# Kernel tuning notes

Measured on AMD Instinct MI355X. Metric: run time of the kernel, lower is better.

Reference implementation:

```python
import jax, jax.numpy as jnp
import numpy as np

N_E = 1024
E_DIM = 64
BETA = 0.25
N_TOK = 262144


def setup_inputs() -> dict:
    key = jax.random.key(0)
    k1, k2 = jax.random.split(key)
    x = jax.random.normal(k1, (N_TOK, E_DIM), dtype=jnp.float32)
    # torch init: uniform(-1/n_e, 1/n_e); use same distribution for the codebook
    codebook = jax.random.uniform(k2, (N_E, E_DIM), dtype=jnp.float32,
                                  minval=-1.0 / N_E, maxval=1.0 / N_E)
    return {"x": x, "codebook": codebook}


def reference(x, codebook):
    latent = x.reshape(-1, E_DIM)                       # [N, e_dim]
    # squared euclidean distances: [N, n_e]
    d = (jnp.sum(latent * latent, axis=1, keepdims=True)
         + jnp.sum(codebook * codebook, axis=1)[None, :]
         - 2.0 * jnp.matmul(latent, codebook.T))
    indices = jnp.argmin(d, axis=-1)                    # [N] int
    x_q = jnp.take(codebook, indices, axis=0).reshape(x.shape)
    # commitment: mse(stop_grad(x_q), x); codebook: mse(x_q, stop_grad(x))
    diff2 = jnp.mean((x_q - x) ** 2)
    loss = diff2 + BETA * diff2  # fwd values identical; grads differ (handled in bwd module)
    # straight-through estimator
    x_q_st = x + jax.lax.stop_gradient(x_q - x)
    return x_q_st, loss, indices.reshape(x.shape[:-1])
```

## Files before the change

### kernel.cpp

```cpp
#include <hip/hip_runtime.h>
#include <float.h>

#define N_TOK 262144
#define N_E   1024
#define E_DIM 64
#define BETA  0.25f

typedef float f32x64 __attribute__((ext_vector_type(64)));

__device__ __forceinline__ float np_sumsq64_v(f32x64 v)
{
    float r0 = __fmul_rn(v[1], v[1]);
    float r1 = __fmul_rn(v[2], v[2]);
    float r2 = __fmul_rn(v[3], v[3]);
    float r3 = __fmul_rn(v[4], v[4]);
    float r4 = __fmul_rn(v[5], v[5]);
    float r5 = __fmul_rn(v[6], v[6]);
    float r6 = __fmul_rn(v[7], v[7]);
    float r7 = __fmul_rn(v[8], v[8]);
#define VQ_ACC8(blk)                                                     \
    r0 = __fadd_rn(r0, __fmul_rn(v[1 + (blk) + 0], v[1 + (blk) + 0]));  \
    r1 = __fadd_rn(r1, __fmul_rn(v[1 + (blk) + 1], v[1 + (blk) + 1]));  \
    r2 = __fadd_rn(r2, __fmul_rn(v[1 + (blk) + 2], v[1 + (blk) + 2]));  \
    r3 = __fadd_rn(r3, __fmul_rn(v[1 + (blk) + 3], v[1 + (blk) + 3]));  \
    r4 = __fadd_rn(r4, __fmul_rn(v[1 + (blk) + 4], v[1 + (blk) + 4]));  \
    r5 = __fadd_rn(r5, __fmul_rn(v[1 + (blk) + 5], v[1 + (blk) + 5]));  \
    r6 = __fadd_rn(r6, __fmul_rn(v[1 + (blk) + 6], v[1 + (blk) + 6]));  \
    r7 = __fadd_rn(r7, __fmul_rn(v[1 + (blk) + 7], v[1 + (blk) + 7]))
    VQ_ACC8(8);
    VQ_ACC8(16);
    VQ_ACC8(24);
    VQ_ACC8(32);
    VQ_ACC8(40);
    VQ_ACC8(48);
#undef VQ_ACC8
    float tA  = __fadd_rn(__fadd_rn(r0, r1), __fadd_rn(r2, r3));
    float tB  = __fadd_rn(__fadd_rn(r4, r5), __fadd_rn(r6, r7));
    float res = __fadd_rn(tA, tB);
    res = __fadd_rn(res, __fmul_rn(v[57], v[57]));
    res = __fadd_rn(res, __fmul_rn(v[58], v[58]));
    res = __fadd_rn(res, __fmul_rn(v[59], v[59]));
    res = __fadd_rn(res, __fmul_rn(v[60], v[60]));
    res = __fadd_rn(res, __fmul_rn(v[61], v[61]));
    res = __fadd_rn(res, __fmul_rn(v[62], v[62]));
    res = __fadd_rn(res, __fmul_rn(v[63], v[63]));
    return __fadd_rn(__fmul_rn(v[0], v[0]), res);
}

__global__ __launch_bounds__(256) void vq_prep(const float* __restrict__ cb,
                                               float* __restrict__ scn,
                                               float* __restrict__ loss_slot)
{
    int j = blockIdx.x * 256 + threadIdx.x;
    if (j < N_E) {
        const float* c = cb + (size_t)j * E_DIM;
        f32x64 cr;
#pragma unroll
        for (int k = 0; k < E_DIM; k += 4) {
            float4 v = *(const float4*)(c + k);
            cr[k] = v.x; cr[k + 1] = v.y; cr[k + 2] = v.z; cr[k + 3] = v.w;
        }
        scn[j] = np_sumsq64_v(cr);
    }
    if (blockIdx.x == 0 && threadIdx.x == 0) *loss_slot = 0.f;
}

__global__ __launch_bounds__(256)
void vq_main(const float* __restrict__ x,
             const float* __restrict__ cb,
             const float* __restrict__ scn,
             float* __restrict__ xq_out,
             float* __restrict__ loss_out,
             float* __restrict__ idx_out)
{
    const int tok = blockIdx.x * blockDim.x + threadIdx.x;

    f32x64 xr;
    {
        const float* xrow = x + (size_t)tok * E_DIM;
#pragma unroll
        for (int k = 0; k < E_DIM; k += 4) {
            float4 v = *(const float4*)(xrow + k);
            xr[k] = v.x; xr[k + 1] = v.y; xr[k + 2] = v.z; xr[k + 3] = v.w;
        }
    }

    const float sx = np_sumsq64_v(xr);

    float dmin = FLT_MAX;
    int   imin = 0;

    for (int j = 0; j < N_E; j += 2) {
        const float* c0 = cb + (size_t)j * E_DIM;
        const float* c1 = c0 + E_DIM;
        float m0 = 0.f, m1 = 0.f;
#pragma unroll
        for (int k = 0; k < E_DIM; ++k) {
            m0 = fmaf(xr[k], c0[k], m0);
            m1 = fmaf(xr[k], c1[k], m1);
        }
        float d0 = __fsub_rn(__fadd_rn(sx, scn[j    ]), __fmul_rn(2.0f, m0));
        float d1 = __fsub_rn(__fadd_rn(sx, scn[j + 1]), __fmul_rn(2.0f, m1));
        if (d0 < dmin) { dmin = d0; imin = j; }
        if (d1 < dmin) { dmin = d1; imin = j + 1; }
    }

    float lsum = 0.f;
    {
        const float* cmin = cb + (size_t)imin * E_DIM;
        float*       xq   = xq_out + (size_t)tok * E_DIM;
#pragma unroll
        for (int k = 0; k < E_DIM; k += 4) {
            float4 cv = *(const float4*)(cmin + k);
            *(float4*)(xq + k) = cv;
            float e0 = cv.x - xr[k    ];
            float e1 = cv.y - xr[k + 1];
            float e2 = cv.z - xr[k + 2];
            float e3 = cv.w - xr[k + 3];
            lsum = fmaf(e0, e0, lsum);
            lsum = fmaf(e1, e1, lsum);
            lsum = fmaf(e2, e2, lsum);
            lsum = fmaf(e3, e3, lsum);
        }
    }
    idx_out[tok] = (float)imin;

    for (int m = 1; m < 64; m <<= 1) lsum += __shfl_xor(lsum, m, 64);
    __shared__ float red[4];
    const int lane = threadIdx.x & 63;
    const int wid  = threadIdx.x >> 6;
    if (lane == 0) red[wid] = lsum;
    __syncthreads();
    if (threadIdx.x == 0) {
        float part = red[0] + red[1] + red[2] + red[3];
        const float scale = (1.0f + BETA) / ((float)N_TOK * (float)E_DIM);
        atomicAdd(loss_out, part * scale);
    }
}

extern "C" void kernel_launch(void* const* d_in, const int* in_sizes, int n_in,
                              void* d_out, int out_size, void* d_ws, size_t ws_size,
                              hipStream_t stream)
{
    const float* x  = (const float*)d_in[0];
    const float* cb = (const float*)d_in[1];

    float* out  = (float*)d_out;
    float* xq   = out;
    float* loss = out + (size_t)N_TOK * E_DIM;
    float* idx  = loss + 1;

    float* scn = (float*)d_ws;

    vq_prep<<<N_E / 256, 256, 0, stream>>>(cb, scn, loss);
    vq_main<<<N_TOK / 256, 256, 0, stream>>>(x, cb, scn, xq, loss, idx);
}
```

Baseline: 614.5 us.

## Stage token rows in shared memory and tile codebook into 16-entry register blocks

Each token's vector now lives in a transposed shared-memory tile instead of 64 registers, and the distance loop computes 16 codebook dot products at once over 16-wide k-chunks. This is meant to free registers for more resident waves and to amortise each x value across 16 codewords, which raises FMA density per load. The block size also drops from 256 to 128. In exchange every x element is re-read from LDS for each codebook tile, and the codebook loads, which are uniform across the wave, become 16 separate scalar or broadcast streams.

```diff
diff --git a/kernel.cpp b/kernel.cpp
--- a/kernel.cpp
+++ b/kernel.cpp
@@ -5,6 +5,8 @@
 #define N_E   1024
 #define E_DIM 64
 #define BETA  0.25f
+#define BLK   128
+#define NTILE 16
 
 typedef float f32x64 __attribute__((ext_vector_type(64)));
 
@@ -19,20 +21,15 @@
     float r6 = __fmul_rn(v[7], v[7]);
     float r7 = __fmul_rn(v[8], v[8]);
 #define VQ_ACC8(blk)                                                     \
-    r0 = __fadd_rn(r0, __fmul_rn(v[1 + (blk) + 0], v[1 + (blk) + 0]));  \
-    r1 = __fadd_rn(r1, __fmul_rn(v[1 + (blk) + 1], v[1 + (blk) + 1]));  \
-    r2 = __fadd_rn(r2, __fmul_rn(v[1 + (blk) + 2], v[1 + (blk) + 2]));  \
-    r3 = __fadd_rn(r3, __fmul_rn(v[1 + (blk) + 3], v[1 + (blk) + 3]));  \
-    r4 = __fadd_rn(r4, __fmul_rn(v[1 + (blk) + 4], v[1 + (blk) + 4]));  \
-    r5 = __fadd_rn(r5, __fmul_rn(v[1 + (blk) + 5], v[1 + (blk) + 5]));  \
-    r6 = __fadd_rn(r6, __fmul_rn(v[1 + (blk) + 6], v[1 + (blk) + 6]));  \
-    r7 = __fadd_rn(r7, __fmul_rn(v[1 + (blk) + 7], v[1 + (blk) + 7]))
-    VQ_ACC8(8);
-    VQ_ACC8(16);
-    VQ_ACC8(24);
-    VQ_ACC8(32);
-    VQ_ACC8(40);
-    VQ_ACC8(48);
+    r0 = __fadd_rn(r0, __fmul_rn(v[1 + (blk)], v[1 + (blk)]));          \
+    r1 = __fadd_rn(r1, __fmul_rn(v[2 + (blk)], v[2 + (blk)]));          \
+    r2 = __fadd_rn(r2, __fmul_rn(v[3 + (blk)], v[3 + (blk)]));          \
+    r3 = __fadd_rn(r3, __fmul_rn(v[4 + (blk)], v[4 + (blk)]));          \
+    r4 = __fadd_rn(r4, __fmul_rn(v[5 + (blk)], v[5 + (blk)]));          \
+    r5 = __fadd_rn(r5, __fmul_rn(v[6 + (blk)], v[6 + (blk)]));          \
+    r6 = __fadd_rn(r6, __fmul_rn(v[7 + (blk)], v[7 + (blk)]));          \
+    r7 = __fadd_rn(r7, __fmul_rn(v[8 + (blk)], v[8 + (blk)]))
+    VQ_ACC8(8); VQ_ACC8(16); VQ_ACC8(24); VQ_ACC8(32); VQ_ACC8(40); VQ_ACC8(48);
 #undef VQ_ACC8
     float tA  = __fadd_rn(__fadd_rn(r0, r1), __fadd_rn(r2, r3));
     float tB  = __fadd_rn(__fadd_rn(r4, r5), __fadd_rn(r6, r7));
@@ -65,7 +62,7 @@
     if (blockIdx.x == 0 && threadIdx.x == 0) *loss_slot = 0.f;
 }
 
-__global__ __launch_bounds__(256)
+__global__ __launch_bounds__(BLK)
 void vq_main(const float* __restrict__ x,
              const float* __restrict__ cb,
              const float* __restrict__ scn,
@@ -73,36 +70,110 @@
              float* __restrict__ loss_out,
              float* __restrict__ idx_out)
 {
-    const int tok = blockIdx.x * blockDim.x + threadIdx.x;
-
-    f32x64 xr;
+    __shared__ float At[E_DIM][BLK];
+    __shared__ float red[2];
+
+    const int t   = threadIdx.x;
+    const int tok = blockIdx.x * BLK + t;
+
+#define XT(k) At[(k)][t]
+
     {
         const float* xrow = x + (size_t)tok * E_DIM;
 #pragma unroll
-        for (int k = 0; k < E_DIM; k += 4) {
-            float4 v = *(const float4*)(xrow + k);
-            xr[k] = v.x; xr[k + 1] = v.y; xr[k + 2] = v.z; xr[k + 3] = v.w;
+        for (int c = 0; c < 16; ++c) {
+            float4 v = *(const float4*)(xrow + 4 * c);
+            At[4 * c + 0][t] = v.x;
+            At[4 * c + 1][t] = v.y;
+            At[4 * c + 2][t] = v.z;
+            At[4 * c + 3][t] = v.w;
         }
     }
 
-    const float sx = np_sumsq64_v(xr);
+    float sx;
+    {
+#define Q(k) __fmul_rn(XT(k), XT(k))
+        float r0 = Q(1), r1 = Q(2), r2 = Q(3), r3 = Q(4);
+        float r4 = Q(5), r5 = Q(6), r6 = Q(7), r7 = Q(8);
+#define SACC(b)                                  \
+        r0 = __fadd_rn(r0, Q(1 + (b)));          \
+        r1 = __fadd_rn(r1, Q(2 + (b)));          \
+        r2 = __fadd_rn(r2, Q(3 + (b)));          \
+        r3 = __fadd_rn(r3, Q(4 + (b)));          \
+        r4 = __fadd_rn(r4, Q(5 + (b)));          \
+        r5 = __fadd_rn(r5, Q(6 + (b)));          \
+        r6 = __fadd_rn(r6, Q(7 + (b)));          \
+        r7 = __fadd_rn(r7, Q(8 + (b)));
+        SACC(8) SACC(16) SACC(24) SACC(32) SACC(40) SACC(48)
+#undef SACC
+        float tA  = __fadd_rn(__fadd_rn(r0, r1), __fadd_rn(r2, r3));
+        float tB  = __fadd_rn(__fadd_rn(r4, r5), __fadd_rn(r6, r7));
+        float res = __fadd_rn(tA, tB);
+        res = __fadd_rn(res, Q(57));
+        res = __fadd_rn(res, Q(58));
+        res = __fadd_rn(res, Q(59));
+        res = __fadd_rn(res, Q(60));
+        res = __fadd_rn(res, Q(61));
+        res = __fadd_rn(res, Q(62));
+        res = __fadd_rn(res, Q(63));
+        sx = __fadd_rn(Q(0), res);
+#undef Q
+    }
 
     float dmin = FLT_MAX;
     int   imin = 0;
 
-    for (int j = 0; j < N_E; j += 2) {
-        const float* c0 = cb + (size_t)j * E_DIM;
-        const float* c1 = c0 + E_DIM;
-        float m0 = 0.f, m1 = 0.f;
-#pragma unroll
-        for (int k = 0; k < E_DIM; ++k) {
-            m0 = fmaf(xr[k], c0[k], m0);
-            m1 = fmaf(xr[k], c1[k], m1);
-        }
-        float d0 = __fsub_rn(__fadd_rn(sx, scn[j    ]), __fmul_rn(2.0f, m0));
-        float d1 = __fsub_rn(__fadd_rn(sx, scn[j + 1]), __fmul_rn(2.0f, m1));
-        if (d0 < dmin) { dmin = d0; imin = j; }
-        if (d1 < dmin) { dmin = d1; imin = j + 1; }
+#define FMAQ(xv, kk, ma, mb, mc, md)             \
+    ma = fmaf(xv, p0[kk], ma);                   \
+    mb = fmaf(xv, p1[kk], mb);                   \
+    mc = fmaf(xv, p2[kk], mc);                   \
+    md = fmaf(xv, p3[kk], md);
+
+#define GROUP(jbase, kc, ma, mb, mc, md) do {                        \
+    const float* p0 = cb + (size_t)(jbase) * E_DIM + (kc);           \
+    const float* p1 = p0 + E_DIM;                                    \
+    const float* p2 = p1 + E_DIM;                                    \
+    const float* p3 = p2 + E_DIM;                                    \
+    FMAQ(x0, 0, ma, mb, mc, md)  FMAQ(x1, 1, ma, mb, mc, md)         \
+    FMAQ(x2, 2, ma, mb, mc, md)  FMAQ(x3, 3, ma, mb, mc, md)         \
+    FMAQ(x4, 4, ma, mb, mc, md)  FMAQ(x5, 5, ma, mb, mc, md)         \
+    FMAQ(x6, 6, ma, mb, mc, md)  FMAQ(x7, 7, ma, mb, mc, md)         \
+    FMAQ(x8, 8, ma, mb, mc, md)  FMAQ(x9, 9, ma, mb, mc, md)         \
+    FMAQ(x10, 10, ma, mb, mc, md) FMAQ(x11, 11, ma, mb, mc, md)      \
+    FMAQ(x12, 12, ma, mb, mc, md) FMAQ(x13, 13, ma, mb, mc, md)      \
+    FMAQ(x14, 14, ma, mb, mc, md) FMAQ(x15, 15, ma, mb, mc, md)      \
+} while (0)
+
+#define CHUNK(kc) do {                                               \
+    const float x0  = XT((kc) + 0),  x1  = XT((kc) + 1);             \
+    const float x2  = XT((kc) + 2),  x3  = XT((kc) + 3);             \
+    const float x4  = XT((kc) + 4),  x5  = XT((kc) + 5);             \
+    const float x6  = XT((kc) + 6),  x7  = XT((kc) + 7);             \
+    const float x8  = XT((kc) + 8),  x9  = XT((kc) + 9);             \
+    const float x10 = XT((kc) + 10), x11 = XT((kc) + 11);            \
+    const float x12 = XT((kc) + 12), x13 = XT((kc) + 13);            \
+    const float x14 = XT((kc) + 14), x15 = XT((kc) + 15);            \
+    GROUP(j0 + 0,  (kc), m00, m01, m02, m03);                        \
+    GROUP(j0 + 4,  (kc), m04, m05, m06, m07);                        \
+    GROUP(j0 + 8,  (kc), m08, m09, m10, m11);                        \
+    GROUP(j0 + 12, (kc), m12, m13, m14, m15);                        \
+} while (0)
+
+#define DCHK(jl, mv) {                                                      \
+    float d = __fsub_rn(__fadd_rn(sx, scn[j0 + (jl)]), __fmul_rn(2.0f, mv)); \
+    if (d < dmin) { dmin = d; imin = j0 + (jl); }                           \
+}
+
+    for (int j0 = 0; j0 < N_E; j0 += NTILE) {
+        float m00 = 0.f, m01 = 0.f, m02 = 0.f, m03 = 0.f;
+        float m04 = 0.f, m05 = 0.f, m06 = 0.f, m07 = 0.f;
+        float m08 = 0.f, m09 = 0.f, m10 = 0.f, m11 = 0.f;
+        float m12 = 0.f, m13 = 0.f, m14 = 0.f, m15 = 0.f;
+        CHUNK(0); CHUNK(16); CHUNK(32); CHUNK(48);
+        DCHK(0, m00)  DCHK(1, m01)  DCHK(2, m02)  DCHK(3, m03)
+        DCHK(4, m04)  DCHK(5, m05)  DCHK(6, m06)  DCHK(7, m07)
+        DCHK(8, m08)  DCHK(9, m09)  DCHK(10, m10) DCHK(11, m11)
+        DCHK(12, m12) DCHK(13, m13) DCHK(14, m14) DCHK(15, m15)
     }
 
     float lsum = 0.f;
@@ -110,13 +181,13 @@
         const float* cmin = cb + (size_t)imin * E_DIM;
         float*       xq   = xq_out + (size_t)tok * E_DIM;
 #pragma unroll
-        for (int k = 0; k < E_DIM; k += 4) {
-            float4 cv = *(const float4*)(cmin + k);
-            *(float4*)(xq + k) = cv;
-            float e0 = cv.x - xr[k    ];
-            float e1 = cv.y - xr[k + 1];
-            float e2 = cv.z - xr[k + 2];
-            float e3 = cv.w - xr[k + 3];
+        for (int c = 0; c < 16; ++c) {
+            float4 cv = *(const float4*)(cmin + 4 * c);
+            *(float4*)(xq + 4 * c) = cv;
+            float e0 = cv.x - XT(4 * c + 0);
+            float e1 = cv.y - XT(4 * c + 1);
+            float e2 = cv.z - XT(4 * c + 2);
+            float e3 = cv.w - XT(4 * c + 3);
             lsum = fmaf(e0, e0, lsum);
             lsum = fmaf(e1, e1, lsum);
             lsum = fmaf(e2, e2, lsum);
@@ -126,16 +197,18 @@
     idx_out[tok] = (float)imin;
 
     for (int m = 1; m < 64; m <<= 1) lsum += __shfl_xor(lsum, m, 64);
-    __shared__ float red[4];
-    const int lane = threadIdx.x & 63;
-    const int wid  = threadIdx.x >> 6;
-    if (lane == 0) red[wid] = lsum;
+    if ((t & 63) == 0) red[t >> 6] = lsum;
     __syncthreads();
-    if (threadIdx.x == 0) {
-        float part = red[0] + red[1] + red[2] + red[3];
+    if (t == 0) {
+        float part = red[0] + red[1];
         const float scale = (1.0f + BETA) / ((float)N_TOK * (float)E_DIM);
         atomicAdd(loss_out, part * scale);
     }
+#undef XT
+#undef FMAQ
+#undef GROUP
+#undef CHUNK
+#undef DCHK
 }
 
 extern "C" void kernel_launch(void* const* d_in, const int* in_sizes, int n_in,
@@ -153,5 +226,5 @@
     float* scn = (float*)d_ws;
 
     vq_prep<<<N_E / 256, 256, 0, stream>>>(cb, scn, loss);
-    vq_main<<<N_TOK / 256, 256, 0, stream>>>(x, cb, scn, xq, loss, idx);
-}
+    vq_main<<<N_TOK / BLK, BLK, 0, stream>>>(x, cb, scn, xq, loss, idx);
+}
```

New measurement: 1.749 ms. 2.85x slower.

## Spill part of token vector to LDS and process four codes per iteration

Applied to the files above, without the earlier changes.

Keeps 40 of the 64 token features in registers and stores the other 24 in a per-thread LDS column. This cuts VGPR pressure so more waves can be resident. The codebook loop now computes four distance dot products per iteration instead of two, amortising the uniform codebook loads. The cost is an LDS read for every FMA on the top 24 features, which adds LDS traffic on the hot path.

```diff
diff --git a/kernel.cpp b/kernel.cpp
--- a/kernel.cpp
+++ b/kernel.cpp
@@ -5,6 +5,9 @@
 #define N_E   1024
 #define E_DIM 64
 #define BETA  0.25f
+#define BLK   256
+#define NREG  40
+#define NLDS  24
 
 typedef float f32x64 __attribute__((ext_vector_type(64)));
 
@@ -19,20 +22,15 @@
     float r6 = __fmul_rn(v[7], v[7]);
     float r7 = __fmul_rn(v[8], v[8]);
 #define VQ_ACC8(blk)                                                     \
-    r0 = __fadd_rn(r0, __fmul_rn(v[1 + (blk) + 0], v[1 + (blk) + 0]));  \
-    r1 = __fadd_rn(r1, __fmul_rn(v[1 + (blk) + 1], v[1 + (blk) + 1]));  \
-    r2 = __fadd_rn(r2, __fmul_rn(v[1 + (blk) + 2], v[1 + (blk) + 2]));  \
-    r3 = __fadd_rn(r3, __fmul_rn(v[1 + (blk) + 3], v[1 + (blk) + 3]));  \
-    r4 = __fadd_rn(r4, __fmul_rn(v[1 + (blk) + 4], v[1 + (blk) + 4]));  \
-    r5 = __fadd_rn(r5, __fmul_rn(v[1 + (blk) + 5], v[1 + (blk) + 5]));  \
-    r6 = __fadd_rn(r6, __fmul_rn(v[1 + (blk) + 6], v[1 + (blk) + 6]));  \
-    r7 = __fadd_rn(r7, __fmul_rn(v[1 + (blk) + 7], v[1 + (blk) + 7]))
-    VQ_ACC8(8);
-    VQ_ACC8(16);
-    VQ_ACC8(24);
-    VQ_ACC8(32);
-    VQ_ACC8(40);
-    VQ_ACC8(48);
+    r0 = __fadd_rn(r0, __fmul_rn(v[1 + (blk)], v[1 + (blk)]));          \
+    r1 = __fadd_rn(r1, __fmul_rn(v[2 + (blk)], v[2 + (blk)]));          \
+    r2 = __fadd_rn(r2, __fmul_rn(v[3 + (blk)], v[3 + (blk)]));          \
+    r3 = __fadd_rn(r3, __fmul_rn(v[4 + (blk)], v[4 + (blk)]));          \
+    r4 = __fadd_rn(r4, __fmul_rn(v[5 + (blk)], v[5 + (blk)]));          \
+    r5 = __fadd_rn(r5, __fmul_rn(v[6 + (blk)], v[6 + (blk)]));          \
+    r6 = __fadd_rn(r6, __fmul_rn(v[7 + (blk)], v[7 + (blk)]));          \
+    r7 = __fadd_rn(r7, __fmul_rn(v[8 + (blk)], v[8 + (blk)]))
+    VQ_ACC8(8); VQ_ACC8(16); VQ_ACC8(24); VQ_ACC8(32); VQ_ACC8(40); VQ_ACC8(48);
 #undef VQ_ACC8
     float tA  = __fadd_rn(__fadd_rn(r0, r1), __fadd_rn(r2, r3));
     float tB  = __fadd_rn(__fadd_rn(r4, r5), __fadd_rn(r6, r7));
@@ -65,7 +63,7 @@
     if (blockIdx.x == 0 && threadIdx.x == 0) *loss_slot = 0.f;
 }
 
-__global__ __launch_bounds__(256)
+__global__ __launch_bounds__(BLK)
 void vq_main(const float* __restrict__ x,
              const float* __restrict__ cb,
              const float* __restrict__ scn,
@@ -73,66 +71,213 @@
              float* __restrict__ loss_out,
              float* __restrict__ idx_out)
 {
-    const int tok = blockIdx.x * blockDim.x + threadIdx.x;
-
-    f32x64 xr;
+    __shared__ float At[NLDS][BLK];
+    __shared__ float red[4];
+
+    const int t   = threadIdx.x;
+    const int tok = blockIdx.x * BLK + t;
+
+    float x0,  x1,  x2,  x3,  x4,  x5,  x6,  x7,  x8,  x9;
+    float x10, x11, x12, x13, x14, x15, x16, x17, x18, x19;
+    float x20, x21, x22, x23, x24, x25, x26, x27, x28, x29;
+    float x30, x31, x32, x33, x34, x35, x36, x37, x38, x39;
+
+#define XV_0 x0
+#define XV_1 x1
+#define XV_2 x2
+#define XV_3 x3
+#define XV_4 x4
+#define XV_5 x5
+#define XV_6 x6
+#define XV_7 x7
+#define XV_8 x8
+#define XV_9 x9
+#define XV_10 x10
+#define XV_11 x11
+#define XV_12 x12
+#define XV_13 x13
+#define XV_14 x14
+#define XV_15 x15
+#define XV_16 x16
+#define XV_17 x17
+#define XV_18 x18
+#define XV_19 x19
+#define XV_20 x20
+#define XV_21 x21
+#define XV_22 x22
+#define XV_23 x23
+#define XV_24 x24
+#define XV_25 x25
+#define XV_26 x26
+#define XV_27 x27
+#define XV_28 x28
+#define XV_29 x29
+#define XV_30 x30
+#define XV_31 x31
+#define XV_32 x32
+#define XV_33 x33
+#define XV_34 x34
+#define XV_35 x35
+#define XV_36 x36
+#define XV_37 x37
+#define XV_38 x38
+#define XV_39 x39
+#define XV_40 At[0][t]
+#define XV_41 At[1][t]
+#define XV_42 At[2][t]
+#define XV_43 At[3][t]
+#define XV_44 At[4][t]
+#define XV_45 At[5][t]
+#define XV_46 At[6][t]
+#define XV_47 At[7][t]
+#define XV_48 At[8][t]
+#define XV_49 At[9][t]
+#define XV_50 At[10][t]
+#define XV_51 At[11][t]
+#define XV_52 At[12][t]
+#define XV_53 At[13][t]
+#define XV_54 At[14][t]
+#define XV_55 At[15][t]
+#define XV_56 At[16][t]
+#define XV_57 At[17][t]
+#define XV_58 At[18][t]
+#define XV_59 At[19][t]
+#define XV_60 At[20][t]
+#define XV_61 At[21][t]
+#define XV_62 At[22][t]
+#define XV_63 At[23][t]
+#define XV(k) XV_##k
+
     {
         const float* xrow = x + (size_t)tok * E_DIM;
-#pragma unroll
-        for (int k = 0; k < E_DIM; k += 4) {
-            float4 v = *(const float4*)(xrow + k);
-            xr[k] = v.x; xr[k + 1] = v.y; xr[k + 2] = v.z; xr[k + 3] = v.w;
-        }
-    }
-
-    const float sx = np_sumsq64_v(xr);
+        float4 q;
+        q = *(const float4*)(xrow +  0); x0  = q.x; x1  = q.y; x2  = q.z; x3  = q.w;
+        q = *(const float4*)(xrow +  4); x4  = q.x; x5  = q.y; x6  = q.z; x7  = q.w;
+        q = *(const float4*)(xrow +  8); x8  = q.x; x9  = q.y; x10 = q.z; x11 = q.w;
+        q = *(const float4*)(xrow + 12); x12 = q.x; x13 = q.y; x14 = q.z; x15 = q.w;
+        q = *(const float4*)(xrow + 16); x16 = q.x; x17 = q.y; x18 = q.z; x19 = q.w;
+        q = *(const float4*)(xrow + 20); x20 = q.x; x21 = q.y; x22 = q.z; x23 = q.w;
+        q = *(const float4*)(xrow + 24); x24 = q.x; x25 = q.y; x26 = q.z; x27 = q.w;
+        q = *(const float4*)(xrow + 28); x28 = q.x; x29 = q.y; x30 = q.z; x31 = q.w;
+        q = *(const float4*)(xrow + 32); x32 = q.x; x33 = q.y; x34 = q.z; x35 = q.w;
+        q = *(const float4*)(xrow + 36); x36 = q.x; x37 = q.y; x38 = q.z; x39 = q.w;
+        q = *(const float4*)(xrow + 40); At[0][t]  = q.x; At[1][t]  = q.y; At[2][t]  = q.z; At[3][t]  = q.w;
+        q = *(const float4*)(xrow + 44); At[4][t]  = q.x; At[5][t]  = q.y; At[6][t]  = q.z; At[7][t]  = q.w;
+        q = *(const float4*)(xrow + 48); At[8][t]  = q.x; At[9][t]  = q.y; At[10][t] = q.z; At[11][t] = q.w;
+        q = *(const float4*)(xrow + 52); At[12][t] = q.x; At[13][t] = q.y; At[14][t] = q.z; At[15][t] = q.w;
+        q = *(const float4*)(xrow + 56); At[16][t] = q.x; At[17][t] = q.y; At[18][t] = q.z; At[19][t] = q.w;
+        q = *(const float4*)(xrow + 60); At[20][t] = q.x; At[21][t] = q.y; At[22][t] = q.z; At[23][t] = q.w;
+    }
+
+    float sx;
+    {
+#define Q(k) __fmul_rn(XV(k), XV(k))
+        float r0 = Q(1), r1 = Q(2), r2 = Q(3), r3 = Q(4);
+        float r4 = Q(5), r5 = Q(6), r6 = Q(7), r7 = Q(8);
+        r0 = __fadd_rn(r0, Q(9));  r1 = __fadd_rn(r1, Q(10));
+        r2 = __fadd_rn(r2, Q(11)); r3 = __fadd_rn(r3, Q(12));
+        r4 = __fadd_rn(r4, Q(13)); r5 = __fadd_rn(r5, Q(14));
+        r6 = __fadd_rn(r6, Q(15)); r7 = __fadd_rn(r7, Q(16));
+        r0 = __fadd_rn(r0, Q(17)); r1 = __fadd_rn(r1, Q(18));
+        r2 = __fadd_rn(r2, Q(19)); r3 = __fadd_rn(r3, Q(20));
+        r4 = __fadd_rn(r4, Q(21)); r5 = __fadd_rn(r5, Q(22));
+        r6 = __fadd_rn(r6, Q(23)); r7 = __fadd_rn(r7, Q(24));
+        r0 = __fadd_rn(r0, Q(25)); r1 = __fadd_rn(r1, Q(26));
+        r2 = __fadd_rn(r2, Q(27)); r3 = __fadd_rn(r3, Q(28));
+        r4 = __fadd_rn(r4, Q(29)); r5 = __fadd_rn(r5, Q(30));
+        r6 = __fadd_rn(r6, Q(31)); r7 = __fadd_rn(r7, Q(32));
+        r0 = __fadd_rn(r0, Q(33)); r1 = __fadd_rn(r1, Q(34));
+        r2 = __fadd_rn(r2, Q(35)); r3 = __fadd_rn(r3, Q(36));
+        r4 = __fadd_rn(r4, Q(37)); r5 = __fadd_rn(r5, Q(38));
+        r6 = __fadd_rn(r6, Q(39)); r7 = __fadd_rn(r7, Q(40));
+        r0 = __fadd_rn(r0, Q(41)); r1 = __fadd_rn(r1, Q(42));
+        r2 = __fadd_rn(r2, Q(43)); r3 = __fadd_rn(r3, Q(44));
+        r4 = __fadd_rn(r4, Q(45)); r5 = __fadd_rn(r5, Q(46));
+        r6 = __fadd_rn(r6, Q(47)); r7 = __fadd_rn(r7, Q(48));
+        r0 = __fadd_rn(r0, Q(49)); r1 = __fadd_rn(r1, Q(50));
+        r2 = __fadd_rn(r2, Q(51)); r3 = __fadd_rn(r3, Q(52));
+        r4 = __fadd_rn(r4, Q(53)); r5 = __fadd_rn(r5, Q(54));
+        r6 = __fadd_rn(r6, Q(55)); r7 = __fadd_rn(r7, Q(56));
+        float tA  = __fadd_rn(__fadd_rn(r0, r1), __fadd_rn(r2, r3));
+        float tB  = __fadd_rn(__fadd_rn(r4, r5), __fadd_rn(r6, r7));
+        float res = __fadd_rn(tA, tB);
+        res = __fadd_rn(res, Q(57));
+        res = __fadd_rn(res, Q(58));
+        res = __fadd_rn(res, Q(59));
+        res = __fadd_rn(res, Q(60));
+        res = __fadd_rn(res, Q(61));
+        res = __fadd_rn(res, Q(62));
+        res = __fadd_rn(res, Q(63));
+        sx = __fadd_rn(Q(0), res);
+#undef Q
+    }
 
     float dmin = FLT_MAX;
     int   imin = 0;
 
-    for (int j = 0; j < N_E; j += 2) {
-        const float* c0 = cb + (size_t)j * E_DIM;
+#define FK(k) {                                   \
+        const float xv = XV(k);                   \
+        m0 = fmaf(xv, c0[k], m0);                 \
+        m1 = fmaf(xv, c1[k], m1);                 \
+        m2 = fmaf(xv, c2[k], m2);                 \
+        m3 = fmaf(xv, c3[k], m3);                 \
+    }
+
+#pragma clang loop unroll(disable)
+    for (int j0 = 0; j0 < N_E; j0 += 4) {
+        const float* c0 = cb + (size_t)j0 * E_DIM;
         const float* c1 = c0 + E_DIM;
-        float m0 = 0.f, m1 = 0.f;
-#pragma unroll
-        for (int k = 0; k < E_DIM; ++k) {
-            m0 = fmaf(xr[k], c0[k], m0);
-            m1 = fmaf(xr[k], c1[k], m1);
-        }
-        float d0 = __fsub_rn(__fadd_rn(sx, scn[j    ]), __fmul_rn(2.0f, m0));
-        float d1 = __fsub_rn(__fadd_rn(sx, scn[j + 1]), __fmul_rn(2.0f, m1));
-        if (d0 < dmin) { dmin = d0; imin = j; }
-        if (d1 < dmin) { dmin = d1; imin = j + 1; }
-    }
+        const float* c2 = c1 + E_DIM;
+        const float* c3 = c2 + E_DIM;
+        float m0 = 0.f, m1 = 0.f, m2 = 0.f, m3 = 0.f;
+        FK(0)  FK(1)  FK(2)  FK(3)  FK(4)  FK(5)  FK(6)  FK(7)
+        FK(8)  FK(9)  FK(10) FK(11) FK(12) FK(13) FK(14) FK(15)
+        FK(16) FK(17) FK(18) FK(19) FK(20) FK(21) FK(22) FK(23)
+        FK(24) FK(25) FK(26) FK(27) FK(28) FK(29) FK(30) FK(31)
+        FK(32) FK(33) FK(34) FK(35) FK(36) FK(37) FK(38) FK(39)
+        FK(40) FK(41) FK(42) FK(43) FK(44) FK(45) FK(46) FK(47)
+        FK(48) FK(49) FK(50) FK(51) FK(52) FK(53) FK(54) FK(55)
+        FK(56) FK(57) FK(58) FK(59) FK(60) FK(61) FK(62) FK(63)
+        float d0 = __fsub_rn(__fadd_rn(sx, scn[j0    ]), __fmul_rn(2.0f, m0));
+        float d1 = __fsub_rn(__fadd_rn(sx, scn[j0 + 1]), __fmul_rn(2.0f, m1));
+        float d2 = __fsub_rn(__fadd_rn(sx, scn[j0 + 2]), __fmul_rn(2.0f, m2));
+        float d3 = __fsub_rn(__fadd_rn(sx, scn[j0 + 3]), __fmul_rn(2.0f, m3));
+        if (d0 < dmin) { dmin = d0; imin = j0; }
+        if (d1 < dmin) { dmin = d1; imin = j0 + 1; }
+        if (d2 < dmin) { dmin = d2; imin = j0 + 2; }
+        if (d3 < dmin) { dmin = d3; imin = j0 + 3; }
+    }
+#undef FK
 
     float lsum = 0.f;
     {
         const float* cmin = cb + (size_t)imin * E_DIM;
         float*       xq   = xq_out + (size_t)tok * E_DIM;
-#pragma unroll
-        for (int k = 0; k < E_DIM; k += 4) {
-            float4 cv = *(const float4*)(cmin + k);
-            *(float4*)(xq + k) = cv;
-            float e0 = cv.x - xr[k    ];
-            float e1 = cv.y - xr[k + 1];
-            float e2 = cv.z - xr[k + 2];
-            float e3 = cv.w - xr[k + 3];
-            lsum = fmaf(e0, e0, lsum);
-            lsum = fmaf(e1, e1, lsum);
-            lsum = fmaf(e2, e2, lsum);
-            lsum = fmaf(e3, e3, lsum);
-        }
+        float4 cv; float e;
+#define LQ(base, a, b, c, d)                                        \
+        cv = *(const float4*)(cmin + (base));                       \
+        *(float4*)(xq + (base)) = cv;                               \
+        e = cv.x - XV(a); lsum = fmaf(e, e, lsum);                  \
+        e = cv.y - XV(b); lsum = fmaf(e, e, lsum);                  \
+        e = cv.z - XV(c); lsum = fmaf(e, e, lsum);                  \
+        e = cv.w - XV(d); lsum = fmaf(e, e, lsum);
+        LQ(0,  0, 1, 2, 3)    LQ(4,  4, 5, 6, 7)
+        LQ(8,  8, 9, 10, 11)  LQ(12, 12, 13, 14, 15)
+        LQ(16, 16, 17, 18, 19) LQ(20, 20, 21, 22, 23)
+        LQ(24, 24, 25, 26, 27) LQ(28, 28, 29, 30, 31)
+        LQ(32, 32, 33, 34, 35) LQ(36, 36, 37, 38, 39)
+        LQ(40, 40, 41, 42, 43) LQ(44, 44, 45, 46, 47)
+        LQ(48, 48, 49, 50, 51) LQ(52, 52, 53, 54, 55)
+        LQ(56, 56, 57, 58, 59) LQ(60, 60, 61, 62, 63)
+#undef LQ
     }
     idx_out[tok] = (float)imin;
 
     for (int m = 1; m < 64; m <<= 1) lsum += __shfl_xor(lsum, m, 64);
-    __shared__ float red[4];
-    const int lane = threadIdx.x & 63;
-    const int wid  = threadIdx.x >> 6;
-    if (lane == 0) red[wid] = lsum;
+    if ((t & 63) == 0) red[t >> 6] = lsum;
     __syncthreads();
-    if (threadIdx.x == 0) {
-        float part = red[0] + red[1] + red[2] + red[3];
+    if (t == 0) {
+        float part = (red[0] + red[1]) + (red[2] + red[3]);
         const float scale = (1.0f + BETA) / ((float)N_TOK * (float)E_DIM);
         atomicAdd(loss_out, part * scale);
     }
@@ -153,5 +298,5 @@
     float* scn = (float*)d_ws;
 
     vq_prep<<<N_E / 256, 256, 0, stream>>>(cb, scn, loss);
-    vq_main<<<N_TOK / 256, 256, 0, stream>>>(x, cb, scn, xq, loss, idx);
+    vq_main<<<N_TOK / BLK, BLK, 0, stream>>>(x, cb, scn, xq, loss, idx);
 }
```

Result: slower. 752.8 us (+22.5%).

## Split codebook search across two thread halves per token block

Applied to the files above, without the earlier changes.

Each block now handles 128 tokens with 256 threads, so every token gets two threads that each scan half of the codebook (512 entries). The upper half writes its local minimum to shared memory, and the lower half merges it and produces the output, index and loss contribution. This halves the serial loop length per thread and doubles the thread count, which is meant to expose more parallelism and hide latency. The cost is redundant loading of x and its norm in both halves and an extra barrier. Tie-breaking still prefers the lower index because the strict-less comparison keeps the first half on equal distances.

```diff
diff --git a/kernel.cpp b/kernel.cpp
--- a/kernel.cpp
+++ b/kernel.cpp
@@ -5,6 +5,9 @@
 #define N_E   1024
 #define E_DIM 64
 #define BETA  0.25f
+#define BLK   256
+#define TPB   128
+#define JSPL  512
 
 typedef float f32x64 __attribute__((ext_vector_type(64)));
 
@@ -19,20 +22,15 @@
     float r6 = __fmul_rn(v[7], v[7]);
     float r7 = __fmul_rn(v[8], v[8]);
 #define VQ_ACC8(blk)                                                     \
-    r0 = __fadd_rn(r0, __fmul_rn(v[1 + (blk) + 0], v[1 + (blk) + 0]));  \
-    r1 = __fadd_rn(r1, __fmul_rn(v[1 + (blk) + 1], v[1 + (blk) + 1]));  \
-    r2 = __fadd_rn(r2, __fmul_rn(v[1 + (blk) + 2], v[1 + (blk) + 2]));  \
-    r3 = __fadd_rn(r3, __fmul_rn(v[1 + (blk) + 3], v[1 + (blk) + 3]));  \
-    r4 = __fadd_rn(r4, __fmul_rn(v[1 + (blk) + 4], v[1 + (blk) + 4]));  \
-    r5 = __fadd_rn(r5, __fmul_rn(v[1 + (blk) + 5], v[1 + (blk) + 5]));  \
-    r6 = __fadd_rn(r6, __fmul_rn(v[1 + (blk) + 6], v[1 + (blk) + 6]));  \
-    r7 = __fadd_rn(r7, __fmul_rn(v[1 + (blk) + 7], v[1 + (blk) + 7]))
-    VQ_ACC8(8);
-    VQ_ACC8(16);
-    VQ_ACC8(24);
-    VQ_ACC8(32);
-    VQ_ACC8(40);
-    VQ_ACC8(48);
+    r0 = __fadd_rn(r0, __fmul_rn(v[1 + (blk)], v[1 + (blk)]));          \
+    r1 = __fadd_rn(r1, __fmul_rn(v[2 + (blk)], v[2 + (blk)]));          \
+    r2 = __fadd_rn(r2, __fmul_rn(v[3 + (blk)], v[3 + (blk)]));          \
+    r3 = __fadd_rn(r3, __fmul_rn(v[4 + (blk)], v[4 + (blk)]));          \
+    r4 = __fadd_rn(r4, __fmul_rn(v[5 + (blk)], v[5 + (blk)]));          \
+    r5 = __fadd_rn(r5, __fmul_rn(v[6 + (blk)], v[6 + (blk)]));          \
+    r6 = __fadd_rn(r6, __fmul_rn(v[7 + (blk)], v[7 + (blk)]));          \
+    r7 = __fadd_rn(r7, __fmul_rn(v[8 + (blk)], v[8 + (blk)]))
+    VQ_ACC8(8); VQ_ACC8(16); VQ_ACC8(24); VQ_ACC8(32); VQ_ACC8(40); VQ_ACC8(48);
 #undef VQ_ACC8
     float tA  = __fadd_rn(__fadd_rn(r0, r1), __fadd_rn(r2, r3));
     float tB  = __fadd_rn(__fadd_rn(r4, r5), __fadd_rn(r6, r7));
@@ -65,7 +63,7 @@
     if (blockIdx.x == 0 && threadIdx.x == 0) *loss_slot = 0.f;
 }
 
-__global__ __launch_bounds__(256)
+__global__ __launch_bounds__(BLK)
 void vq_main(const float* __restrict__ x,
              const float* __restrict__ cb,
              const float* __restrict__ scn,
@@ -73,7 +71,15 @@
              float* __restrict__ loss_out,
              float* __restrict__ idx_out)
 {
-    const int tok = blockIdx.x * blockDim.x + threadIdx.x;
+    __shared__ float md[TPB];
+    __shared__ int   mi[TPB];
+    __shared__ float red[4];
+
+    const int t    = threadIdx.x;
+    const int half = t >> 7;
+    const int lt   = t & (TPB - 1);
+    const int tok  = blockIdx.x * TPB + lt;
+    const int jb   = half * JSPL;
 
     f32x64 xr;
     {
@@ -88,9 +94,9 @@
     const float sx = np_sumsq64_v(xr);
 
     float dmin = FLT_MAX;
-    int   imin = 0;
+    int   imin = jb;
 
-    for (int j = 0; j < N_E; j += 2) {
+    for (int j = jb; j < jb + JSPL; j += 2) {
         const float* c0 = cb + (size_t)j * E_DIM;
         const float* c1 = c0 + E_DIM;
         float m0 = 0.f, m1 = 0.f;
@@ -105,8 +111,14 @@
         if (d1 < dmin) { dmin = d1; imin = j + 1; }
     }
 
+    if (half) { md[lt] = dmin; mi[lt] = imin; }
+    __syncthreads();
+
     float lsum = 0.f;
-    {
+    if (!half) {
+        float dh = md[lt]; int ih = mi[lt];
+        if (dh < dmin) { dmin = dh; imin = ih; }
+
         const float* cmin = cb + (size_t)imin * E_DIM;
         float*       xq   = xq_out + (size_t)tok * E_DIM;
 #pragma unroll
@@ -122,17 +134,14 @@
             lsum = fmaf(e2, e2, lsum);
             lsum = fmaf(e3, e3, lsum);
         }
+        idx_out[tok] = (float)imin;
     }
-    idx_out[tok] = (float)imin;
 
     for (int m = 1; m < 64; m <<= 1) lsum += __shfl_xor(lsum, m, 64);
-    __shared__ float red[4];
-    const int lane = threadIdx.x & 63;
-    const int wid  = threadIdx.x >> 6;
-    if (lane == 0) red[wid] = lsum;
+    if ((t & 63) == 0) red[t >> 6] = lsum;
     __syncthreads();
-    if (threadIdx.x == 0) {
-        float part = red[0] + red[1] + red[2] + red[3];
+    if (t == 0) {
+        float part = (red[0] + red[1]) + (red[2] + red[3]);
         const float scale = (1.0f + BETA) / ((float)N_TOK * (float)E_DIM);
         atomicAdd(loss_out, part * scale);
     }
@@ -153,5 +162,5 @@
     float* scn = (float*)d_ws;
 
     vq_prep<<<N_E / 256, 256, 0, stream>>>(cb, scn, loss);
-    vq_main<<<N_TOK / 256, 256, 0, stream>>>(x, cb, scn, xq, loss, idx);
+    vq_main<<<N_TOK / TPB, BLK, 0, stream>>>(x, cb, scn, xq, loss, idx);
 }
```

Result: slower. 1.888 ms (+207.2%).
